# Kernel tuning notes

Hardware: AMD Instinct MI355X
Metric: run time of the kernel (lower is better)

## Reference

```python
import jax, jax.numpy as jnp
import numpy as np

V = 8000      # output_size (vocab)
EMB = 256     # emb_size
ENC = 512     # enc_hid_size
DEC = 512     # dec_hid_size
HE = 20       # energizer hidden (fixed in source)


def setup_inputs() -> dict:
    key = jax.random.key(0)
    ks = jax.random.split(key, 12)
    B, S, T = 64, 128, 128
    s = 0.05
    return {
        "enc_hid": jax.random.normal(ks[0], (B, S, ENC), dtype=jnp.float32),
        "real_output": jax.random.randint(ks[1], (B, T), 0, V),
        "W_e1": jax.random.normal(ks[2], (ENC + DEC, HE), dtype=jnp.float32) * s,
        "b_e1": jnp.zeros((HE,), jnp.float32),
        "W_e2": jax.random.normal(ks[3], (HE, 1), dtype=jnp.float32) * s,
        "b_e2": jnp.zeros((1,), jnp.float32),
        "emb": jax.random.normal(ks[4], (V, EMB), dtype=jnp.float32) * s,
        "W_rnn": jax.random.normal(ks[5], (EMB + DEC + ENC, DEC), dtype=jnp.float32) * s,
        "b_rnn": jnp.zeros((DEC,), jnp.float32),
        "W_out": jax.random.normal(ks[6], (EMB + DEC + ENC, V), dtype=jnp.float32) * s,
        "b_out": jnp.zeros((V,), jnp.float32),
    }


def _decode(enc_hid, real_output, W_e1, b_e1, W_e2, b_e2, emb, W_rnn, b_rnn, W_out, b_out):
    B, S, _ = enc_hid.shape

    def step(carry, y_i):
        last_char, last_hidden = carry  # [B] int, [B,DEC]
        # additive attention, vectorized over all encoder positions
        hid_b = jnp.broadcast_to(last_hidden[:, None, :], (B, S, DEC))
        cat = jnp.concatenate([enc_hid, hid_b], axis=-1)          # [B,S,ENC+DEC]
        e = jax.nn.elu(cat @ W_e1 + b_e1)                          # [B,S,HE]
        e = jax.nn.elu(e @ W_e2 + b_e2)[..., 0]                    # [B,S]
        ew = jnp.exp(e)
        w = ew / jnp.sum(ew, axis=1, keepdims=True)                # [B,S]
        context = jnp.einsum('bs,bse->be', w, enc_hid)             # [B,ENC]
        last_ch = emb[last_char % V]                               # [B,EMB]
        new_hidden = jax.nn.elu(
            jnp.concatenate([last_ch, last_hidden, context], axis=1) @ W_rnn + b_rnn)
        out = jax.nn.elu(
            jnp.concatenate([last_ch, new_hidden, context], axis=1) @ W_out + b_out)
        # teacher_forcing_prob = 1.0 -> next char is the ground truth token
        return (y_i, new_hidden), (out, w)

    init = (jnp.zeros((B,), real_output.dtype), jnp.zeros((B, DEC), enc_hid.dtype))
    _, (outs, weights) = jax.lax.scan(step, init, real_output.T)   # [T,B,V], [T,B,S]
    return outs.transpose(1, 0, 2), weights.transpose(1, 0, 2)


def reference(enc_hid, real_output, W_e1, b_e1, W_e2, b_e2, emb, W_rnn, b_rnn, W_out, b_out):
    return _decode(enc_hid, real_output, W_e1, b_e1, W_e2, b_e2, emb,
                   W_rnn, b_rnn, W_out, b_out)
```

## Files before the change

kernel.cpp:

```cpp
#include <hip/hip_runtime.h>
#include <hip/hip_bf16.h>
#include <stdint.h>

#define BATCH 64
#define SLEN 128
#define TLEN 128
#define ENCD 512
#define DECD 512
#define EMBD 256
#define VOC  8000
#define HE   20
#define KX   1280
#define NPAD 8064

typedef __attribute__((ext_vector_type(8))) short short8;
typedef __attribute__((ext_vector_type(8))) _Float16 half8v;
typedef __attribute__((ext_vector_type(4))) float f32x4;
typedef _Float16 h2 __attribute__((ext_vector_type(2)));

__device__ inline unsigned short f2bf(float f) {
  union { float f; uint32_t u; } v; v.f = f;
  uint32_t r = v.u + 0x7fff + ((v.u >> 16) & 1);
  return (unsigned short)(r >> 16);
}
__device__ inline unsigned short f16bits(float f) {
  union { _Float16 h; unsigned short u; } c; c.h = (_Float16)f; return c.u;
}
__device__ inline uint32_t pkh2(float a, float b) {
  union { h2 h; uint32_t u; } v;
  v.h = h2{(_Float16)a, (_Float16)b};
  return v.u;
}
__device__ inline float fdot2(uint32_t a, uint32_t b, float c) {
#if __has_builtin(__builtin_amdgcn_fdot2)
  union { uint32_t u; h2 h; } x, y; x.u = a; y.u = b;
  return __builtin_amdgcn_fdot2(x.h, y.h, c, false);
#else
  union { uint32_t u; h2 h; } x, y; x.u = a; y.u = b;
  return c + (float)x.h[0] * (float)y.h[0] + (float)x.h[1] * (float)y.h[1];
#endif
}
__device__ inline float eluf(float x) { return x > 0.f ? x : (expf(x) - 1.f); }

typedef const __attribute__((address_space(1))) unsigned int* gptr_t;
typedef __attribute__((address_space(3))) unsigned int* lptr_t;
__device__ inline void gload16(const void* g, void* l) {
  __builtin_amdgcn_global_load_lds((gptr_t)g, (lptr_t)l, 16, 0, 0);
}

__global__ __launch_bounds__(256) void k_pre1(const int* __restrict__ ro,
                                              const float* __restrict__ emb,
                                              unsigned short* __restrict__ X,
                                              const float* __restrict__ enc,
                                              unsigned short* __restrict__ ench,
                                              const float* __restrict__ We1,
                                              float* __restrict__ E1) {
  __shared__ float rowbuf[4][ENCD];
  __shared__ float part[4][HE][2];
  int bid = blockIdx.x, tid = threadIdx.x;
  if (bid < 8192) {
    int r = bid;
    int t = r >> 6, b = r & 63;
    int lc = (t == 0) ? 0 : ro[b * TLEN + t - 1];
    lc = ((lc % VOC) + VOC) % VOC;
    X[(size_t)r * KX + tid] = f2bf(emb[(size_t)lc * EMBD + tid]);
  } else if (bid < 12288) {
    int i = ((bid - 8192) * 256 + tid) * 4;
    float4 v = *(const float4*)(enc + i);
    ushort4 o = { f16bits(v.x), f16bits(v.y), f16bits(v.z), f16bits(v.w) };
    *(ushort4*)(ench + i) = o;
  } else {
    int r0 = (bid - 12288) * 4;
    for (int i = tid; i < 4 * ENCD; i += 256) {
      int rl = i >> 9, e = i & 511;
      rowbuf[rl][e] = enc[(size_t)(r0 + rl) * ENCD + e];
    }
    __syncthreads();
    if (tid < 160) {
      int kg = tid / 80, rem = tid % 80, rl = rem / 20, h = rem % 20;
      float acc = 0.f;
      for (int k = kg * 256; k < kg * 256 + 256; ++k)
        acc += rowbuf[rl][k] * We1[k * HE + h];
      part[rl][h][kg] = acc;
    }
    __syncthreads();
    if (tid < 80) {
      int rl = tid / 20, h = tid % 20;
      int r = r0 + rl, bb = r >> 7, ss = r & 127;
      E1[((size_t)bb * HE + h) * SLEN + ss] = part[rl][h][0] + part[rl][h][1];
    }
  }
}

__global__ __launch_bounds__(256) void k_pre2(const float* __restrict__ Wr,
                                              unsigned short* __restrict__ WembT,
                                              unsigned short* __restrict__ WctxT,
                                              unsigned short* __restrict__ W2) {
  __shared__ float tile[64][65];
  int bid = blockIdx.x, tid = threadIdx.x;
  if (bid < 96) {
    int k0, KN, fmt, bx, by;
    unsigned short* dst;
    if (bid < 32) { k0 = 0;   KN = 256; fmt = 1; bx = bid & 7; by = bid >> 3; dst = WembT; }
    else          { int id2 = bid - 32; k0 = 768; KN = 512; fmt = 0; bx = id2 & 7; by = id2 >> 3; dst = WctxT; }
    int n0 = bx * 64, kt = by * 64;
    for (int i = tid; i < 4096; i += 256) {
      int kk = i >> 6, nn = i & 63;
      tile[kk][nn] = Wr[(size_t)(k0 + kt + kk) * 512 + n0 + nn];
    }
    __syncthreads();
    for (int i = tid; i < 4096; i += 256) {
      int nn = i >> 6, kk = i & 63;
      float v = tile[kk][nn];
      dst[(size_t)(n0 + nn) * KN + kt + kk] = fmt ? f2bf(v) : f16bits(v);
    }
  } else {
    int i = (bid - 96) * 256 + tid;
    int n = i & 511;
    int j = (i >> 9) & 7;
    int kc = (i >> 12) & 31;
    int h = (i >> 17) & 1;
    int k = h * 256 + kc * 8 + j;
    W2[(((size_t)(h * 32 + kc) * 512) + n) * 8 + j] = f16bits(Wr[(size_t)(256 + k) * 512 + n]);
  }
}

__global__ __launch_bounds__(256) void k_wh(const float* __restrict__ wout,
                                            unsigned short* __restrict__ wh) {
  int i = (blockIdx.x * 256 + threadIdx.x) * 4;
  float4 v = *(const float4*)(wout + i);
  ushort4 o = { f16bits(v.x), f16bits(v.y), f16bits(v.z), f16bits(v.w) };
  *(ushort4*)(wh + i) = o;
}

#define BM 128
#define BN 128
#define BK 64

template<int MODE>
__global__ __launch_bounds__(256) void k_gs(
    const unsigned short* __restrict__ A,
    const unsigned short* __restrict__ B,
    const float* __restrict__ bias,
    unsigned short* __restrict__ Cout)
{
  constexpr int As = (MODE == 0) ? KX : (MODE == 1 ? 512 : 128);
  constexpr int Bs = (MODE == 0) ? 256 : (MODE == 1 ? 512 : 128);
  constexpr int KT = (MODE == 0) ? 4 : (MODE == 1 ? 8 : 2);
  __shared__ __align__(16) unsigned short Asd[BM * BK];
  __shared__ __align__(16) unsigned short Bsd[BN * BK];
  int bx = blockIdx.x, by = blockIdx.y;
  int tid = threadIdx.x;
  int wid = tid >> 6, lane = tid & 63;
  int wr = wid >> 1, wc = wid & 1;

  f32x4 acc[4][4];
  for (int i = 0; i < 4; ++i)
    for (int j = 0; j < 4; ++j) acc[i][j] = (f32x4)0.f;

  const unsigned short* Abase = A + (size_t)by * BM * As;
  const unsigned short* Bbase = B + (size_t)bx * BN * Bs + (MODE == 2 ? (size_t)by * 512 * 128 : 0);

  for (int kt = 0; kt < KT; ++kt) {
    for (int j = 0; j < 4; ++j) {
      int c = tid + j * 256;
      int r = c >> 3, c16 = c & 7;
      int sk = c16 ^ (r & 7);
      gload16(Abase + (size_t)r * As + kt * BK + sk * 8, (char*)Asd + c * 16);
      gload16(Bbase + (size_t)r * Bs + kt * BK + sk * 8, (char*)Bsd + c * 16);
    }
    __syncthreads();
    for (int ks = 0; ks < 2; ++ks) {
      short8 af[4], bf[4];
      int kc = ks * 4 + (lane >> 4);
      for (int i = 0; i < 4; ++i) {
        int r = wr * 64 + i * 16 + (lane & 15);
        af[i] = *(const short8*)((const char*)Asd + r * 128 + ((kc ^ (r & 7)) * 16));
      }
      for (int j = 0; j < 4; ++j) {
        int r = wc * 64 + j * 16 + (lane & 15);
        bf[j] = *(const short8*)((const char*)Bsd + r * 128 + ((kc ^ (r & 7)) * 16));
      }
      for (int i = 0; i < 4; ++i)
        for (int j = 0; j < 4; ++j) {
          if constexpr (MODE == 0)
            acc[i][j] = __builtin_amdgcn_mfma_f32_16x16x32_bf16(af[i], bf[j], acc[i][j], 0, 0, 0);
          else
            acc[i][j] = __builtin_amdgcn_mfma_f32_16x16x32_f16(
                __builtin_bit_cast(half8v, af[i]), __builtin_bit_cast(half8v, bf[j]), acc[i][j], 0, 0, 0);
        }
    }
    __syncthreads();
  }

  int rl = lane >> 4, cl = lane & 15;
  for (int j = 0; j < 4; ++j) {
    int gn = bx * BN + wc * 64 + j * 16 + cl;
    for (int i = 0; i < 4; ++i) {
      for (int q = 0; q < 4; ++q) {
        int gm = by * BM + wr * 64 + i * 16 + rl * 4 + q;
        float v = acc[i][j][q];
        if constexpr (MODE == 0) {
          Cout[(size_t)gm * 512 + gn] = f16bits(v + bias[gn]);
        } else if constexpr (MODE == 1) {
          int bb = gm >> 7, s = gm & 127;
          Cout[(((size_t)(bb * 16 + (s >> 3)) * 512) + gn) * 8 + (s & 7)] = f16bits(v);
        } else {
          int tt = gm & 127, bb = gm >> 7;
          Cout[((size_t)tt * 64 + bb) * KX + 768 + gn] = f2bf(v);
        }
      }
    }
  }
}

#define STREAM4(PH) { \
  float a0 = 0, a1 = 0, a2 = 0, a3 = 0; \
  uint4 cb[8], nb[8]; \
  _Pragma("unroll") \
  for (int j = 0; j < 8; ++j) cb[j] = Wp[(size_t)j * 512]; \
  for (int blk = 0; blk < 4; ++blk) { \
    if (blk + 1 < 4) { \
      _Pragma("unroll") \
      for (int j = 0; j < 8; ++j) nb[j] = Wp[(size_t)((blk + 1) * 8 + j) * 512]; \
    } \
    _Pragma("unroll") \
    for (int j = 0; j < 8; ++j) { \
      uint4 wv = cb[j]; uint4 xv = hp4[hbase + blk * 8 + j]; \
      a0 = fdot2(wv.x, xv.x, a0); a1 = fdot2(wv.y, xv.y, a1); \
      a2 = fdot2(wv.z, xv.z, a2); a3 = fdot2(wv.w, xv.w, a3); \
    } \
    _Pragma("unroll") \
    for (int j = 0; j < 8; ++j) cb[j] = nb[j]; \
  } \
  ph[PH][mn] = (a0 + a1) + (a2 + a3); }

__global__ __launch_bounds__(1024) void k_recur(
    const float* __restrict__ We1,
    const float* __restrict__ be1,
    const float* __restrict__ We2,
    const float* __restrict__ be2,
    const uint4* __restrict__ W2,
    const uint4* __restrict__ encW2,
    const unsigned short* __restrict__ Remb,
    const float* __restrict__ E1g,
    unsigned short* __restrict__ X,
    float* __restrict__ wout,
    const float* __restrict__ Wo,
    unsigned short* __restrict__ WoT,
    const float* __restrict__ enc,
    unsigned short* __restrict__ encTh)
{
  __shared__ __align__(16) uint4 el[16][512];
  __shared__ uint32_t E1p[HE][SLEN / 2];
  __shared__ uint32_t w1p[HE][257];
  __shared__ uint32_t hpair[DECD / 2];
  __shared__ uint32_t wpairS[SLEN / 2];
  __shared__ float ph[2][DECD];
  __shared__ float be1s[HE], w2s[HE];
  __shared__ float be2s;

  int bid = blockIdx.x, tid = threadIdx.x;

  if (bid >= 64) {
    float (*tile)[65] = (float(*)[65])el;
    if (bid < 694) {
      for (int q = 0; q < 4; ++q) {
        int t4 = (bid - 64) * 4 + q;
        int n0 = (t4 % 126) * 64, k0 = (t4 / 126) * 64;
        for (int i = tid; i < 4096; i += 1024) {
          int kk = i >> 6, nn = i & 63;
          int n = n0 + nn;
          tile[kk][nn] = (n < VOC) ? Wo[(size_t)(k0 + kk) * VOC + n] : 0.f;
        }
        __syncthreads();
        for (int i = tid; i < 4096; i += 1024) {
          int nn = i >> 6, kk = i & 63;
          WoT[(size_t)(n0 + nn) * KX + k0 + kk] = f2bf(tile[kk][nn]);
        }
        __syncthreads();
      }
    } else {
      for (int q = 0; q < 4; ++q) {
        int t4 = (bid - 694) * 4 + q;
        int eb_ = t4 >> 4;
        int e0 = ((t4 >> 1) & 7) * 64;
        int s0 = (t4 & 1) * 64;
        const float* ebp = enc + (size_t)eb_ * SLEN * ENCD;
        for (int i = tid; i < 4096; i += 1024) {
          int ss = i >> 6, ee = i & 63;
          tile[ss][ee] = ebp[(size_t)(s0 + ss) * ENCD + e0 + ee];
        }
        __syncthreads();
        unsigned short* ob = encTh + (size_t)eb_ * ENCD * SLEN;
        for (int i = tid; i < 4096; i += 1024) {
          int ee = i >> 6, ss = i & 63;
          ob[(size_t)(e0 + ee) * SLEN + s0 + ss] = f16bits(tile[ss][ee]);
        }
        __syncthreads();
      }
    }
    return;
  }

  int b = bid;

  for (int i = tid; i < 16 * 512; i += 1024) ((uint4*)el)[i] = encW2[(size_t)b * 8192 + i];
  for (int i = tid; i < HE * (SLEN / 2); i += 1024) {
    int h = i >> 6, p = i & 63;
    const float* ebase = E1g + ((size_t)b * HE + h) * SLEN;
    ((uint32_t*)E1p)[i] = pkh2(ebase[2 * p], ebase[2 * p + 1]);
  }
  for (int i = tid; i < HE * 256; i += 1024) {
    int h = i >> 8, p = i & 255;
    w1p[h][p] = pkh2(We1[(size_t)(ENCD + 2 * p) * HE + h],
                     We1[(size_t)(ENCD + 2 * p + 1) * HE + h]);
  }
  for (int i = tid; i < DECD / 2; i += 1024) hpair[i] = 0;
  for (int i = tid; i < DECD; i += 1024) { ph[0][i] = 0.f; ph[1][i] = 0.f; }
  if (tid < HE) { be1s[tid] = be1[tid]; w2s[tid] = We2[tid]; }
  if (tid == 0) be2s = be2[0];
  __syncthreads();

  const int lane = tid & 63;
  const int wv_ = tid >> 6;
  int mn, mh0;
  if (tid < 448)      { mn = tid;        mh0 = 0; }
  else if (tid < 896) { mn = tid - 448;  mh0 = 1; }
  else if (tid < 960) { mn = 448 + lane; mh0 = 0; }
  else                { mn = 448 + lane; mh0 = 1; }
  const uint4* Wp = W2 + (size_t)(mh0 * 32) * 512 + mn;
  const uint4* hp4 = (const uint4*)hpair;
  const int hbase = mh0 * 32;

  int ah = lane % 20, aseg = lane / 20;
  int q0 = aseg * 86;
  int q1 = (aseg == 2) ? 256 : q0 + 86;
  if (aseg >= 3) { q0 = 0; q1 = 0; }

  for (int t = 0; t < TLEN; ++t) {
    const int rowr = t * BATCH + b;
    float rpre = 0.f;

    if (wv_ < 15) {
      if (tid < 512) {
        union { unsigned short u; _Float16 f; } c;
        c.u = Remb[(size_t)rowr * 512 + tid];
        rpre = (float)c.f;
      }
      STREAM4(mh0)
    } else {
      __builtin_amdgcn_s_setprio(1);
      float p0 = 0, p1 = 0;
      for (int q = q0; q < q1; q += 2) {
        p0 = fdot2(w1p[ah][q], hpair[q], p0);
        p1 = fdot2(w1p[ah][q + 1], hpair[q + 1], p1);
      }
      float p = p0 + p1;
      float pa = __shfl(p, lane + 20);
      float pb = __shfl(p, lane + 40);
      float edv = p + pa + pb + ((lane < HE) ? be1s[lane] : 0.f);
      float e0a = 0.f, e1a = 0.f;
      #pragma unroll
      for (int h = 0; h < HE; ++h) {
        union { uint32_t u; h2 hh; } e; e.u = E1p[h][lane];
        float ed = __shfl(edv, h);
        e0a += eluf((float)e.hh[0] + ed) * w2s[h];
        e1a += eluf((float)e.hh[1] + ed) * w2s[h];
      }
      float s0 = expf(eluf(e0a + be2s));
      float s1 = expf(eluf(e1a + be2s));
      float tot = s0 + s1;
      #pragma unroll
      for (int o = 1; o < 64; o <<= 1) tot += __shfl_xor(tot, o);
      float inv = 1.f / tot;
      float w0 = s0 * inv, w1 = s1 * inv;
      wpairS[lane] = pkh2(w0, w1);
      float2 wv2 = { w0, w1 };
      *(float2*)(wout + ((size_t)b * TLEN + t) * SLEN + 2 * lane) = wv2;
      __builtin_amdgcn_s_setprio(0);
      STREAM4(1)
    }
    __syncthreads();

    if (tid < 512) {
      int n = tid;
      float c0 = 0, c1 = 0, c2 = 0, c3 = 0;
      #pragma unroll
      for (int g = 0; g < 16; ++g) {
        uint4 ev = el[g][n];
        uint4 wv = ((const uint4*)wpairS)[g];
        c0 = fdot2(ev.x, wv.x, c0); c1 = fdot2(ev.y, wv.y, c1);
        c2 = fdot2(ev.z, wv.z, c2); c3 = fdot2(ev.w, wv.w, c3);
      }
      float v = rpre + ph[0][n] + ph[1][n] + (c0 + c1) + (c2 + c3);
      float aa = eluf(v);
      X[(size_t)rowr * KX + 256 + n] = f2bf(aa);
      float bb = __shfl_down(aa, 1);
      if (!(n & 1)) hpair[n >> 1] = pkh2(aa, bb);
    }
    __syncthreads();
  }
}

__global__ __launch_bounds__(256) void k_gemm(
    const unsigned short* __restrict__ Xb,
    const unsigned short* __restrict__ WoT,
    const float* __restrict__ bout,
    float* __restrict__ out)
{
  __shared__ __align__(16) unsigned short As[BM * BK];
  __shared__ __align__(16) unsigned short Bs[BN * BK];
  int bid = blockIdx.x;
  int swz = (bid & 7) * 504 + (bid >> 3);
  int bx = swz % 63;
  int by = swz / 63;
  int tid = threadIdx.x;
  int wid = tid >> 6, lane = tid & 63;
  int wr = wid >> 1, wc = wid & 1;

  f32x4 acc[4][4];
  for (int i = 0; i < 4; ++i)
    for (int j = 0; j < 4; ++j) acc[i][j] = (f32x4)0.f;

  const unsigned short* Abase = Xb + (size_t)by * BM * KX;
  const unsigned short* Bbase = WoT + (size_t)bx * BN * KX;

  for (int kt = 0; kt < KX / BK; ++kt) {
    for (int j = 0; j < 4; ++j) {
      int c = tid + j * 256;
      int r = c >> 3, c16 = c & 7;
      int sk = c16 ^ (r & 7);
      gload16(Abase + (size_t)r * KX + kt * BK + sk * 8, (char*)As + c * 16);
      gload16(Bbase + (size_t)r * KX + kt * BK + sk * 8, (char*)Bs + c * 16);
    }
    __syncthreads();
    for (int ks = 0; ks < 2; ++ks) {
      short8 af[4], bf[4];
      int kc = ks * 4 + (lane >> 4);
      for (int i = 0; i < 4; ++i) {
        int r = wr * 64 + i * 16 + (lane & 15);
        af[i] = *(const short8*)((const char*)As + r * 128 + ((kc ^ (r & 7)) * 16));
      }
      for (int j = 0; j < 4; ++j) {
        int r = wc * 64 + j * 16 + (lane & 15);
        bf[j] = *(const short8*)((const char*)Bs + r * 128 + ((kc ^ (r & 7)) * 16));
      }
      for (int i = 0; i < 4; ++i)
        for (int j = 0; j < 4; ++j)
          acc[i][j] = __builtin_amdgcn_mfma_f32_16x16x32_bf16(af[i], bf[j], acc[i][j], 0, 0, 0);
    }
    __syncthreads();
  }

  int rl = lane >> 4, cl = lane & 15;
  for (int j = 0; j < 4; ++j) {
    int gn = bx * BN + wc * 64 + j * 16 + cl;
    if (gn >= VOC) continue;
    float bv = bout[gn];
    for (int i = 0; i < 4; ++i) {
      for (int q = 0; q < 4; ++q) {
        int gm = by * BM + wr * 64 + i * 16 + rl * 4 + q;
        int tt = gm >> 6, bb = gm & 63;
        float v = acc[i][j][q] + bv;
        v = v > 0.f ? v : (expf(v) - 1.f);
        out[((size_t)bb * TLEN + tt) * VOC + gn] = v;
      }
    }
  }
}

extern "C" void kernel_launch(void* const* d_in, const int* in_sizes, int n_in,
                              void* d_out, int out_size, void* d_ws, size_t ws_size,
                              hipStream_t stream) {
  const float* enc  = (const float*)d_in[0];
  const int*   ro   = (const int*)d_in[1];
  const float* We1  = (const float*)d_in[2];
  const float* be1  = (const float*)d_in[3];
  const float* We2  = (const float*)d_in[4];
  const float* be2  = (const float*)d_in[5];
  const float* emb  = (const float*)d_in[6];
  const float* Wr   = (const float*)d_in[7];
  const float* brnn = (const float*)d_in[8];
  const float* Wo   = (const float*)d_in[9];
  const float* bo   = (const float*)d_in[10];

  char* ws = (char*)d_ws;
  unsigned short* X     = (unsigned short*)(ws);
  unsigned short* WoT   = (unsigned short*)(ws + 20971520);
  unsigned short* W2    = (unsigned short*)(ws + 41615360);
  unsigned short* WembT = (unsigned short*)(ws + 42139648);
  unsigned short* WctxT = (unsigned short*)(ws + 42401792);
  unsigned short* ench  = (unsigned short*)(ws + 42926080);
  float*          E1    = (float*)(ws + 51314688);
  unsigned short* Remb  = (unsigned short*)(ws + 51970048);
  unsigned short* encW2 = (unsigned short*)(ws + 60358656);
  unsigned short* encTh = ench;
  unsigned short* wh    = Remb;

  float* outs = (float*)d_out;
  float* wout = (float*)d_out + (size_t)BATCH * TLEN * VOC;

  k_pre1 <<<dim3(14336),  256, 0, stream>>>(ro, emb, X, enc, ench, We1, E1);
  k_pre2 <<<dim3(1120),   256, 0, stream>>>(Wr, WembT, WctxT, W2);
  k_gs<0><<<dim3(4, 64),  256, 0, stream>>>(X, WembT, brnn, Remb);
  k_gs<1><<<dim3(4, 64),  256, 0, stream>>>(ench, WctxT, brnn, encW2);
  k_recur<<<dim3(950),   1024, 0, stream>>>(We1, be1, We2, be2,
                                            (const uint4*)W2, (const uint4*)encW2,
                                            Remb, E1, X, wout,
                                            Wo, WoT, enc, encTh);
  k_wh   <<<dim3(1024),   256, 0, stream>>>(wout, wh);
  k_gs<2><<<dim3(4, 64),  256, 0, stream>>>(wh, encTh, brnn, X);
  k_gemm <<<dim3(4032),   256, 0, stream>>>(X, WoT, bo, outs);
  (void)in_sizes; (void)n_in; (void)out_size; (void)ws_size;
}
```

Measured before the change: 1.256 ms.

## Rewrite output GEMM with 256x256 tiles and double-buffered LDS pipeline

The final vocab-projection GEMM moves from 128x128 tiles with 256 threads to 256x256 tiles with 512 threads. It adds double-buffered shared memory so the next K-tile's global loads overlap MFMA work, using explicit waitcnt, barriers and setprio. The padded weight transpose widens from 8064 to 8192 columns so the tile count divides evenly, which shifts the workspace offsets and adds blocks to k_recur. The larger tile cuts global reloads but uses 128KB of LDS and many accumulator registers, so occupancy drops and the padding adds wasted columns.

New measurement: 1.190 ms. 5.3% less time.

```diff
diff --git a/kernel.cpp b/kernel.cpp
--- a/kernel.cpp
+++ b/kernel.cpp
@@ -11,7 +11,7 @@
 #define VOC  8000
 #define HE   20
 #define KX   1280
-#define NPAD 8064
+#define NP2  8192
 
 typedef __attribute__((ext_vector_type(8))) short short8;
 typedef __attribute__((ext_vector_type(8))) _Float16 half8v;
@@ -264,10 +264,10 @@
 
   if (bid >= 64) {
     float (*tile)[65] = (float(*)[65])el;
-    if (bid < 694) {
+    if (bid < 704) {
       for (int q = 0; q < 4; ++q) {
         int t4 = (bid - 64) * 4 + q;
-        int n0 = (t4 % 126) * 64, k0 = (t4 / 126) * 64;
+        int n0 = (t4 % 128) * 64, k0 = (t4 / 128) * 64;
         for (int i = tid; i < 4096; i += 1024) {
           int kk = i >> 6, nn = i & 63;
           int n = n0 + nn;
@@ -282,7 +282,7 @@
       }
     } else {
       for (int q = 0; q < 4; ++q) {
-        int t4 = (bid - 694) * 4 + q;
+        int t4 = (bid - 704) * 4 + q;
         int eb_ = t4 >> 4;
         int e0 = ((t4 >> 1) & 7) * 64;
         int s0 = (t4 & 1) * 64;
@@ -403,64 +403,128 @@
   }
 }
 
-__global__ __launch_bounds__(256) void k_gemm(
+#define GSTAGE(KT, C) { _Pragma("unroll") \
+  for (int j5 = 0; j5 < 4; ++j5) { \
+    int c4 = tid + j5 * 512; \
+    int r5 = c4 >> 3, c16 = c4 & 7; \
+    int sk = c16 ^ (r5 & 7); \
+    gload16(Abase + (size_t)r5 * KX + (KT) * 64 + sk * 8, (char*)Ah[C] + c4 * 16); \
+  } \
+  _Pragma("unroll") \
+  for (int j5 = 0; j5 < 4; ++j5) { \
+    int c4 = tid + j5 * 512; \
+    int r5 = c4 >> 3, c16 = c4 & 7; \
+    int sk = c16 ^ (r5 & 7); \
+    gload16(Bbase + (size_t)r5 * KX + (KT) * 64 + sk * 8, (char*)Bh[C] + c4 * 16); \
+  } }
+
+__global__ __launch_bounds__(512) void k_gemm(
     const unsigned short* __restrict__ Xb,
     const unsigned short* __restrict__ WoT,
     const float* __restrict__ bout,
     float* __restrict__ out)
 {
-  __shared__ __align__(16) unsigned short As[BM * BK];
-  __shared__ __align__(16) unsigned short Bs[BN * BK];
+  __shared__ __align__(16) unsigned short Ah[2][256 * 64];
+  __shared__ __align__(16) unsigned short Bh[2][256 * 64];
   int bid = blockIdx.x;
-  int swz = (bid & 7) * 504 + (bid >> 3);
-  int bx = swz % 63;
-  int by = swz / 63;
+  int swz = (bid & 7) * 128 + (bid >> 3);
+  int by = swz >> 5, bx = swz & 31;
   int tid = threadIdx.x;
-  int wid = tid >> 6, lane = tid & 63;
-  int wr = wid >> 1, wc = wid & 1;
-
-  f32x4 acc[4][4];
-  for (int i = 0; i < 4; ++i)
+  int lane = tid & 63;
+  int wid = tid >> 6;
+  int wrow = wid >> 2, wcol = wid & 3;
+
+  const unsigned short* Abase = Xb + (size_t)by * 256 * KX;
+  const unsigned short* Bbase = WoT + (size_t)bx * 256 * KX;
+
+  f32x4 acc[8][4];
+  #pragma unroll
+  for (int i = 0; i < 8; ++i)
+    #pragma unroll
     for (int j = 0; j < 4; ++j) acc[i][j] = (f32x4)0.f;
 
-  const unsigned short* Abase = Xb + (size_t)by * BM * KX;
-  const unsigned short* Bbase = WoT + (size_t)bx * BN * KX;
-
-  for (int kt = 0; kt < KX / BK; ++kt) {
-    for (int j = 0; j < 4; ++j) {
-      int c = tid + j * 256;
-      int r = c >> 3, c16 = c & 7;
-      int sk = c16 ^ (r & 7);
-      gload16(Abase + (size_t)r * KX + kt * BK + sk * 8, (char*)As + c * 16);
-      gload16(Bbase + (size_t)r * KX + kt * BK + sk * 8, (char*)Bs + c * 16);
-    }
-    __syncthreads();
-    for (int ks = 0; ks < 2; ++ks) {
-      short8 af[4], bf[4];
-      int kc = ks * 4 + (lane >> 4);
-      for (int i = 0; i < 4; ++i) {
-        int r = wr * 64 + i * 16 + (lane & 15);
-        af[i] = *(const short8*)((const char*)As + r * 128 + ((kc ^ (r & 7)) * 16));
-      }
-      for (int j = 0; j < 4; ++j) {
-        int r = wc * 64 + j * 16 + (lane & 15);
-        bf[j] = *(const short8*)((const char*)Bs + r * 128 + ((kc ^ (r & 7)) * 16));
-      }
-      for (int i = 0; i < 4; ++i)
-        for (int j = 0; j < 4; ++j)
-          acc[i][j] = __builtin_amdgcn_mfma_f32_16x16x32_bf16(af[i], bf[j], acc[i][j], 0, 0, 0);
-    }
-    __syncthreads();
+  GSTAGE(0, 0)
+  GSTAGE(1, 1)
+  asm volatile("s_waitcnt vmcnt(8)" ::: "memory");
+  __builtin_amdgcn_s_barrier();
+  __builtin_amdgcn_sched_barrier(0);
+
+  for (int kt = 0; kt < 20; ++kt) {
+    int c = kt & 1;
+    const char* Ab = (const char*)Ah[c];
+    const char* Bb = (const char*)Bh[c];
+    short8 af[4][2], bf[4][2];
+    #pragma unroll
+    for (int i = 0; i < 4; ++i)
+      #pragma unroll
+      for (int ks = 0; ks < 2; ++ks) {
+        int rw = wrow * 128 + i * 16 + (lane & 15);
+        int kc = ks * 4 + (lane >> 4);
+        af[i][ks] = *(const short8*)(Ab + rw * 128 + ((kc ^ (rw & 7)) * 16));
+      }
+    #pragma unroll
+    for (int j = 0; j < 4; ++j)
+      #pragma unroll
+      for (int ks = 0; ks < 2; ++ks) {
+        int rb = wcol * 64 + j * 16 + (lane & 15);
+        int kc = ks * 4 + (lane >> 4);
+        bf[j][ks] = *(const short8*)(Bb + rb * 128 + ((kc ^ (rb & 7)) * 16));
+      }
+    __builtin_amdgcn_s_setprio(1);
+    #pragma unroll
+    for (int i = 0; i < 4; ++i)
+      #pragma unroll
+      for (int j = 0; j < 4; ++j)
+        #pragma unroll
+        for (int ks = 0; ks < 2; ++ks)
+          acc[i][j] = __builtin_amdgcn_mfma_f32_16x16x32_bf16(af[i][ks], bf[j][ks], acc[i][j], 0, 0, 0);
+    __builtin_amdgcn_s_setprio(0);
+    #pragma unroll
+    for (int i = 0; i < 4; ++i)
+      #pragma unroll
+      for (int ks = 0; ks < 2; ++ks) {
+        int rw = wrow * 128 + 64 + i * 16 + (lane & 15);
+        int kc = ks * 4 + (lane >> 4);
+        af[i][ks] = *(const short8*)(Ab + rw * 128 + ((kc ^ (rw & 7)) * 16));
+      }
+    __builtin_amdgcn_s_setprio(1);
+    #pragma unroll
+    for (int i = 0; i < 4; ++i)
+      #pragma unroll
+      for (int j = 0; j < 2; ++j)
+        #pragma unroll
+        for (int ks = 0; ks < 2; ++ks)
+          acc[4 + i][j] = __builtin_amdgcn_mfma_f32_16x16x32_bf16(af[i][ks], bf[j][ks], acc[4 + i][j], 0, 0, 0);
+    __builtin_amdgcn_s_setprio(0);
+    __builtin_amdgcn_s_barrier();
+    __builtin_amdgcn_sched_barrier(0);
+    if (kt < 18) GSTAGE(kt + 2, c)
+    __builtin_amdgcn_s_setprio(1);
+    #pragma unroll
+    for (int i = 0; i < 4; ++i)
+      #pragma unroll
+      for (int j = 0; j < 2; ++j)
+        #pragma unroll
+        for (int ks = 0; ks < 2; ++ks)
+          acc[4 + i][2 + j] = __builtin_amdgcn_mfma_f32_16x16x32_bf16(af[i][ks], bf[2 + j][ks], acc[4 + i][2 + j], 0, 0, 0);
+    __builtin_amdgcn_s_setprio(0);
+    if (kt < 18) { asm volatile("s_waitcnt vmcnt(8)" ::: "memory"); }
+    else         { asm volatile("s_waitcnt vmcnt(0)" ::: "memory"); }
+    __builtin_amdgcn_s_barrier();
+    __builtin_amdgcn_sched_barrier(0);
   }
 
   int rl = lane >> 4, cl = lane & 15;
+  #pragma unroll
   for (int j = 0; j < 4; ++j) {
-    int gn = bx * BN + wc * 64 + j * 16 + cl;
+    int gn = bx * 256 + wcol * 64 + j * 16 + cl;
     if (gn >= VOC) continue;
     float bv = bout[gn];
-    for (int i = 0; i < 4; ++i) {
+    #pragma unroll
+    for (int i = 0; i < 8; ++i) {
+      #pragma unroll
       for (int q = 0; q < 4; ++q) {
-        int gm = by * BM + wr * 64 + i * 16 + rl * 4 + q;
+        int gm = by * 256 + wrow * 128 + i * 16 + rl * 4 + q;
         int tt = gm >> 6, bb = gm & 63;
         float v = acc[i][j][q] + bv;
         v = v > 0.f ? v : (expf(v) - 1.f);
@@ -488,13 +552,13 @@
   char* ws = (char*)d_ws;
   unsigned short* X     = (unsigned short*)(ws);
   unsigned short* WoT   = (unsigned short*)(ws + 20971520);
-  unsigned short* W2    = (unsigned short*)(ws + 41615360);
-  unsigned short* WembT = (unsigned short*)(ws + 42139648);
-  unsigned short* WctxT = (unsigned short*)(ws + 42401792);
-  unsigned short* ench  = (unsigned short*)(ws + 42926080);
-  float*          E1    = (float*)(ws + 51314688);
-  unsigned short* Remb  = (unsigned short*)(ws + 51970048);
-  unsigned short* encW2 = (unsigned short*)(ws + 60358656);
+  unsigned short* W2    = (unsigned short*)(ws + 41943040);
+  unsigned short* WembT = (unsigned short*)(ws + 42467328);
+  unsigned short* WctxT = (unsigned short*)(ws + 42729472);
+  unsigned short* ench  = (unsigned short*)(ws + 43253760);
+  float*          E1    = (float*)(ws + 51642368);
+  unsigned short* Remb  = (unsigned short*)(ws + 52297728);
+  unsigned short* encW2 = (unsigned short*)(ws + 60686336);
   unsigned short* encTh = ench;
   unsigned short* wh    = Remb;
 
@@ -505,12 +569,12 @@
   k_pre2 <<<dim3(1120),   256, 0, stream>>>(Wr, WembT, WctxT, W2);
   k_gs<0><<<dim3(4, 64),  256, 0, stream>>>(X, WembT, brnn, Remb);
   k_gs<1><<<dim3(4, 64),  256, 0, stream>>>(ench, WctxT, brnn, encW2);
-  k_recur<<<dim3(950),   1024, 0, stream>>>(We1, be1, We2, be2,
+  k_recur<<<dim3(960),   1024, 0, stream>>>(We1, be1, We2, be2,
                                             (const uint4*)W2, (const uint4*)encW2,
                                             Remb, E1, X, wout,
                                             Wo, WoT, enc, encTh);
   k_wh   <<<dim3(1024),   256, 0, stream>>>(wout, wh);
   k_gs<2><<<dim3(4, 64),  256, 0, stream>>>(wh, encTh, brnn, X);
-  k_gemm <<<dim3(4032),   256, 0, stream>>>(X, WoT, bo, outs);
+  k_gemm <<<dim3(1024),   512, 0, stream>>>(X, WoT, bo, outs);
   (void)in_sizes; (void)n_in; (void)out_size; (void)ws_size;
 }
```
